# Kernel optimization log

Hardware: AMD Instinct MI355X
Metric: run time of the kernel (lower is better)

## Reference

```python
import jax, jax.numpy as jnp
import numpy as np

B, S, D = 4, 2048, 2048
NQ, NKV = 16, 4
HD = D // NQ          # head_size = 128
GROUP = NQ // NKV     # 4


def _rope_table(seq_len, head_size, theta=10000.0):
    # [seq, head_size/2, 2] = (cos, sin), matching torch polar freqs_cis
    inv = 1.0 / (theta ** (np.arange(0, head_size, 2, dtype=np.float32) / head_size))
    ang = np.arange(seq_len, dtype=np.float32)[:, None] * inv[None, :]
    return jnp.asarray(np.stack([np.cos(ang), np.sin(ang)], axis=-1))


def setup_inputs() -> dict:
    key = jax.random.key(0)
    ks = jax.random.split(key, 6)
    sd = 0.02
    return {
        "x": jax.random.normal(ks[0], (B, S, D), jnp.float32),
        "freq_cis": _rope_table(S, HD),
        "Wq": jax.random.normal(ks[1], (D, NQ * HD), jnp.float32) * sd,
        "bq": jnp.zeros((NQ * HD,), jnp.float32),
        "Wk": jax.random.normal(ks[2], (D, NKV * HD), jnp.float32) * sd,
        "bk": jnp.zeros((NKV * HD,), jnp.float32),
        "Wv": jax.random.normal(ks[3], (D, NKV * HD), jnp.float32) * sd,
        "bv": jnp.zeros((NKV * HD,), jnp.float32),
        "Wo": jax.random.normal(ks[4], (NQ * HD, D), jnp.float32) * sd,
        "start_pos": 0,
    }


def _apply_rope(x, fc):
    # x: [b, s, h, d]; fc: [s, d/2, 2] -> complex multiply on (even, odd) pairs
    xr = x.reshape(*x.shape[:-1], -1, 2)
    cos = fc[None, :, None, :, 0]
    sin = fc[None, :, None, :, 1]
    x0, x1 = xr[..., 0], xr[..., 1]
    out = jnp.stack([x0 * cos - x1 * sin, x0 * sin + x1 * cos], axis=-1)
    return out.reshape(x.shape)


def reference(x, freq_cis, Wq, bq, Wk, bk, Wv, bv, Wo, start_pos):
    b, s, _ = x.shape
    q = (x @ Wq + bq).reshape(b, s, NQ, HD)
    k = (x @ Wk + bk).reshape(b, s, NKV, HD)
    v = (x @ Wv + bv).reshape(b, s, NKV, HD)

    fc = freq_cis[start_pos:start_pos + s]
    q = _apply_rope(q, fc)
    k = _apply_rope(k, fc)

    # [b, nkv, group, s, d] query view; k/v stay [b, nkv, s, d] (GQA broadcast)
    q = q.transpose(0, 2, 1, 3).reshape(b, NKV, GROUP, s, HD)
    k = k.transpose(0, 2, 1, 3)
    v = v.transpose(0, 2, 1, 3)

    scale = 1.0 / jnp.sqrt(jnp.asarray(HD, x.dtype))
    scores = jnp.einsum("bhgqd,bhkd->bhgqk", q, k) * scale
    causal = jnp.tril(jnp.ones((s, s), bool))
    scores = jnp.where(causal[None, None, None], scores, jnp.asarray(-jnp.inf, scores.dtype))
    probs = jax.nn.softmax(scores, axis=-1)
    o = jnp.einsum("bhgqk,bhkd->bhgqd", probs, v)

    o = o.reshape(b, NQ, s, HD).transpose(0, 2, 1, 3).reshape(b, s, NQ * HD)
    return o @ Wo
```

## Files before the change

kernel.cpp:

```cpp
#include <hip/hip_runtime.h>
#include <stdint.h>

typedef __attribute__((ext_vector_type(8))) short bf16x8;
typedef __attribute__((ext_vector_type(4))) float f32x4;
typedef __attribute__((ext_vector_type(16))) float f32x16;

#define S_LEN 2048
#define D_MODEL 2048
#define NQH 16
#define NKVH 4
#define HDIM 128
#define BATCH 4

__device__ __forceinline__ float bf2f(unsigned short s) {
  union { unsigned u; float f; } v; v.u = ((unsigned)s) << 16; return v.f;
}
__device__ __forceinline__ unsigned short f2bf(float f) {
  union { float f; unsigned u; } v; v.f = f;
  unsigned r = v.u + 0x7FFFu + ((v.u >> 16) & 1u);
  return (unsigned short)(r >> 16);
}
__device__ __forceinline__ f32x4 fzero() {
  f32x4 v; v[0]=0.f; v[1]=0.f; v[2]=0.f; v[3]=0.f; return v;
}
__device__ __forceinline__ void async16(const void* g, void* l) {
  __builtin_amdgcn_global_load_lds(
      (const __attribute__((address_space(1))) unsigned int*)g,
      (__attribute__((address_space(3))) unsigned int*)l, 16, 0, 0);
}
__device__ __forceinline__ unsigned cvtpk(float lo, float hi) {
  unsigned r;
  asm("v_cvt_pk_bf16_f32 %0, %1, %2" : "=v"(r) : "v"(lo), "v"(hi));
  return r;
}

__global__ void k_convert_x(const float* __restrict__ x, unsigned short* __restrict__ xb, int n4) {
  int stride = gridDim.x * blockDim.x;
  for (int i = blockIdx.x * blockDim.x + threadIdx.x; i < n4; i += stride) {
    float4 v = ((const float4*)x)[i];
    ushort4 o;
    o.x = f2bf(v.x); o.y = f2bf(v.y); o.z = f2bf(v.z); o.w = f2bf(v.w);
    ((ushort4*)xb)[i] = o;
  }
}

__global__ void k_transpose_convert(const float* __restrict__ W, unsigned short* __restrict__ Wt,
                                    int K, int N) {
  __shared__ float tile[32][33];
  int tx = threadIdx.x & 31, ty = threadIdx.x >> 5;
  int n0 = blockIdx.x * 32, k0 = blockIdx.y * 32;
  #pragma unroll
  for (int i = 0; i < 4; ++i)
    tile[ty + i*8][tx] = W[(size_t)(k0 + ty + i*8) * N + n0 + tx];
  __syncthreads();
  #pragma unroll
  for (int i = 0; i < 4; ++i)
    Wt[(size_t)(n0 + ty + i*8) * K + k0 + tx] = f2bf(tile[tx][ty + i*8]);
}

__global__ void k_transpose_bf16(const unsigned short* __restrict__ src,
                                 unsigned short* __restrict__ dst, int R, int C) {
  __shared__ unsigned short tile[32][33];
  int tx = threadIdx.x & 31, ty = threadIdx.x >> 5;
  int c0 = blockIdx.x * 32, r0 = blockIdx.y * 32;
  const unsigned short* s = src + (size_t)blockIdx.z * R * C;
  unsigned short* d = dst + (size_t)blockIdx.z * R * C;
  #pragma unroll
  for (int i = 0; i < 4; ++i)
    tile[ty + i*8][tx] = s[(size_t)(r0 + ty + i*8) * C + c0 + tx];
  __syncthreads();
  #pragma unroll
  for (int i = 0; i < 4; ++i)
    d[(size_t)(c0 + ty + i*8) * R + r0 + tx] = tile[tx][ty + i*8];
}

__global__ void k_rope(unsigned short* __restrict__ T, const float* __restrict__ fc,
                       const int* __restrict__ start_pos, int total) {
  int sp = start_pos[0];
  int stride = gridDim.x * blockDim.x;
  for (int i = blockIdx.x * blockDim.x + threadIdx.x; i < total; i += stride) {
    int d2 = i & 63;
    int s = (i >> 6) & (S_LEN - 1);
    unsigned v = ((const unsigned*)T)[i];
    float x0 = bf2f((unsigned short)(v & 0xFFFFu));
    float x1 = bf2f((unsigned short)(v >> 16));
    float c  = fc[((size_t)(sp + s) * 64 + d2) * 2];
    float sn = fc[((size_t)(sp + s) * 64 + d2) * 2 + 1];
    float y0 = x0 * c - x1 * sn;
    float y1 = x0 * sn + x1 * c;
    ((unsigned*)T)[i] = (unsigned)f2bf(y0) | ((unsigned)f2bf(y1) << 16);
  }
}


__device__ __forceinline__ bf16x8 ldsrd(const unsigned short* L, int row, int kk, int g) {
  int Xs = (kk * 64 + g * 16) ^ ((row & 7) << 4);
  return *(const bf16x8*)&L[row * 64 + (Xs >> 1)];
}
__device__ __forceinline__ void stage8(const unsigned short* __restrict__ G, int gbase,
                                       int k0, unsigned short* lds, int rowbase, int lane) {
  int row = rowbase + (lane >> 3);
  int col8 = (lane & 7) ^ ((lane >> 3) & 7);
  async16(G + (size_t)(gbase + row) * 2048 + k0 + col8 * 8, lds + rowbase * 64 + lane * 8);
}

#define BARRIER() __builtin_amdgcn_s_barrier()
#define LGKM0()  do { asm volatile("s_waitcnt lgkmcnt(0)" ::: "memory"); \
                      __builtin_amdgcn_sched_barrier(0); } while (0)
#define VMCNT4() asm volatile("s_waitcnt vmcnt(4)" ::: "memory")

template<int EPI>
__global__ __launch_bounds__(512, 2) void k_gemm256(
    const unsigned short* __restrict__ A, const unsigned short* __restrict__ Bt,
    const float* __restrict__ bq, const float* __restrict__ bk, const float* __restrict__ bv,
    unsigned short* __restrict__ Qo, unsigned short* __restrict__ Ko, unsigned short* __restrict__ Vo,
    float* __restrict__ Cf, int NXT)
{
  __shared__ __align__(16) unsigned short Abuf[2][256 * 64];
  __shared__ __align__(16) unsigned short Bbuf[2][256 * 64];
  const int NT = 32;
  const int tid = threadIdx.x, lane = tid & 63, w = tid >> 6;
  const int lr = lane & 15, g = lane >> 4;
  const int wm = w >> 2, wn = w & 3;

  int nwg = NXT * 32;
  int cpx = nwg >> 3;
  int bid = blockIdx.x;
  int swz = (bid & 7) * cpx + (bid >> 3);
  const int by = swz / NXT, bx = swz % NXT;
  const int mbase = by * 256, nbase = bx * 256;

  #define ST_AQ02(tt) if ((tt) < NT) { unsigned short* L = Abuf[(tt) & 1]; int k0 = (tt) * 64; \
    _Pragma("unroll") for (int it = 0; it < 2; ++it) { int sub = it * 8 + w; \
      stage8(A, mbase, k0, L, (sub >> 3) * 128 + (sub & 7) * 8, lane); } }
  #define ST_AQ13(tt) if ((tt) < NT) { unsigned short* L = Abuf[(tt) & 1]; int k0 = (tt) * 64; \
    _Pragma("unroll") for (int it = 0; it < 2; ++it) { int sub = it * 8 + w; \
      stage8(A, mbase, k0, L, 64 + (sub >> 3) * 128 + (sub & 7) * 8, lane); } }
  #define ST_BS0(tt) if ((tt) < NT) { unsigned short* L = Bbuf[(tt) & 1]; int k0 = (tt) * 64; \
    _Pragma("unroll") for (int it = 0; it < 2; ++it) { int sub = it * 8 + w; \
      stage8(Bt, nbase, k0, L, (sub >> 2) * 64 + (sub & 3) * 8, lane); } }
  #define ST_BS1(tt) if ((tt) < NT) { unsigned short* L = Bbuf[(tt) & 1]; int k0 = (tt) * 64; \
    _Pragma("unroll") for (int it = 0; it < 2; ++it) { int sub = it * 8 + w; \
      stage8(Bt, nbase, k0, L, 32 + (sub >> 2) * 64 + (sub & 3) * 8, lane); } }

  f32x4 acc[8][4];
  #pragma unroll
  for (int m = 0; m < 8; ++m)
    #pragma unroll
    for (int n = 0; n < 4; ++n) acc[m][n] = fzero();

  ST_AQ02(0); ST_AQ13(0); ST_BS0(0); ST_BS1(0);
  ST_AQ02(1); ST_BS1(1);
  VMCNT4();
  BARRIER();

  bf16x8 a[2][4], b[2][2];

  for (int t = 0; t < NT; ++t) {
    const unsigned short* Al = Abuf[t & 1];
    const unsigned short* Bl = Bbuf[t & 1];

    #pragma unroll
    for (int kk = 0; kk < 2; ++kk) {
      #pragma unroll
      for (int m = 0; m < 4; ++m) a[kk][m] = ldsrd(Al, wm * 128 + m * 16 + lr, kk, g);
      #pragma unroll
      for (int n = 0; n < 2; ++n) b[kk][n] = ldsrd(Bl, wn * 64 + n * 16 + lr, kk, g);
    }
    ST_AQ13(t + 1);
    BARRIER(); LGKM0();
    __builtin_amdgcn_s_setprio(1);
    #pragma unroll
    for (int kk = 0; kk < 2; ++kk)
      #pragma unroll
      for (int m = 0; m < 4; ++m)
        #pragma unroll
        for (int n = 0; n < 2; ++n)
          acc[m][n] = __builtin_amdgcn_mfma_f32_16x16x32_bf16(a[kk][m], b[kk][n], acc[m][n], 0, 0, 0);
    __builtin_amdgcn_s_setprio(0);
    BARRIER();

    #pragma unroll
    for (int kk = 0; kk < 2; ++kk)
      #pragma unroll
      for (int n = 0; n < 2; ++n) b[kk][n] = ldsrd(Bl, wn * 64 + (2 + n) * 16 + lr, kk, g);
    ST_BS0(t + 1);
    BARRIER(); LGKM0();
    __builtin_amdgcn_s_setprio(1);
    #pragma unroll
    for (int kk = 0; kk < 2; ++kk)
      #pragma unroll
      for (int m = 0; m < 4; ++m)
        #pragma unroll
        for (int n = 0; n < 2; ++n)
          acc[m][2 + n] = __builtin_amdgcn_mfma_f32_16x16x32_bf16(a[kk][m], b[kk][n], acc[m][2 + n], 0, 0, 0);
    __builtin_amdgcn_s_setprio(0);
    BARRIER();

    #pragma unroll
    for (int kk = 0; kk < 2; ++kk)
      #pragma unroll
      for (int m = 0; m < 4; ++m) a[kk][m] = ldsrd(Al, wm * 128 + 64 + m * 16 + lr, kk, g);
    ST_AQ02(t + 2);
    BARRIER(); LGKM0();
    __builtin_amdgcn_s_setprio(1);
    #pragma unroll
    for (int kk = 0; kk < 2; ++kk)
      #pragma unroll
      for (int m = 0; m < 4; ++m)
        #pragma unroll
        for (int n = 0; n < 2; ++n)
          acc[4 + m][2 + n] = __builtin_amdgcn_mfma_f32_16x16x32_bf16(a[kk][m], b[kk][n], acc[4 + m][2 + n], 0, 0, 0);
    __builtin_amdgcn_s_setprio(0);
    BARRIER();

    #pragma unroll
    for (int kk = 0; kk < 2; ++kk)
      #pragma unroll
      for (int n = 0; n < 2; ++n) b[kk][n] = ldsrd(Bl, wn * 64 + n * 16 + lr, kk, g);
    ST_BS1(t + 2);
    VMCNT4();
    BARRIER(); LGKM0();
    __builtin_amdgcn_s_setprio(1);
    #pragma unroll
    for (int kk = 0; kk < 2; ++kk)
      #pragma unroll
      for (int m = 0; m < 4; ++m)
        #pragma unroll
        for (int n = 0; n < 2; ++n)
          acc[4 + m][n] = __builtin_amdgcn_mfma_f32_16x16x32_bf16(a[kk][m], b[kk][n], acc[4 + m][n], 0, 0, 0);
    __builtin_amdgcn_s_setprio(0);
    BARRIER();
  }

  #pragma unroll
  for (int m = 0; m < 8; ++m)
    #pragma unroll
    for (int n = 0; n < 4; ++n)
      #pragma unroll
      for (int i = 0; i < 4; ++i) {
        int mg = mbase + wm * 128 + m * 16 + g * 4 + i;
        int ng = nbase + wn * 64 + n * 16 + lr;
        float val = acc[m][n][i];
        if (EPI == 1) {
          Cf[(size_t)mg * 2048 + ng] = val;
        } else {
          int bb = mg >> 11, s = mg & 2047;
          if (ng < 2048) {
            val += bq[ng];
            int h = ng >> 7, d = ng & 127;
            Qo[((size_t)(bb * NQH + h) * S_LEN + s) * HDIM + d] = f2bf(val);
          } else if (ng < 2560) {
            int nn = ng - 2048;
            val += bk[nn];
            int h = nn >> 7, d = nn & 127;
            Ko[((size_t)(bb * NKVH + h) * S_LEN + s) * HDIM + d] = f2bf(val);
          } else {
            int nn = ng - 2560;
            val += bv[nn];
            int h = nn >> 7, d = nn & 127;
            Vo[((size_t)(bb * NKVH + h) * S_LEN + s) * HDIM + d] = f2bf(val);
          }
        }
      }
  #undef ST_AQ02
  #undef ST_AQ13
  #undef ST_BS0
  #undef ST_BS1
}

__global__ __launch_bounds__(512, 2) void k_flash2(
    const unsigned short* __restrict__ Q, const unsigned short* __restrict__ K,
    const unsigned short* __restrict__ Vt, unsigned short* __restrict__ O)
{
  __shared__ __align__(16) unsigned short SH[32768];

  const int tid = threadIdx.x;
  const int lane = tid & 63;
  const int w = tid >> 6;
  const int ql = lane & 31;
  const int hi = lane >> 5;

  const int bh = blockIdx.x >> 2;
  const int tp = blockIdx.x & 3;
  const int b = bh >> 4, h = bh & 15;
  const int kh = h >> 2;

  const unsigned short* Qbase = Q + (size_t)(b * NQH + h) * S_LEN * HDIM;
  const unsigned short* Kbase = K + (size_t)(b * NKVH + kh) * S_LEN * HDIM;
  const unsigned short* Vtb   = Vt + (size_t)(b * NKVH + kh) * HDIM * S_LEN;

  const float scale = 0.08838834764831845f;

  #pragma unroll 1
  for (int half = 0; half < 2; ++half) {
    const int t = half ? (7 - tp) : tp;
    const int nkv = 4 * t + 4;
    const int qg = t * 256 + w * 32 + ql;

    __syncthreads();

    bf16x8 qf[8];
    {
      const unsigned short* qp = Qbase + (size_t)qg * HDIM;
      #pragma unroll
      for (int dd = 0; dd < 8; ++dd)
        qf[dd] = *(const bf16x8*)(qp + dd * 16 + hi * 8);
    }

    float m_r = -1e30f, l_r = 0.f;
    f32x16 oA[4];
    #pragma unroll
    for (int db = 0; db < 4; ++db)
      #pragma unroll
      for (int r = 0; r < 16; ++r) oA[db][r] = 0.f;

    {
      unsigned short* Kd = SH;
      unsigned short* Vd = SH + 16384;
      #pragma unroll
      for (int it = 0; it < 2; ++it) {
        int c = tid + it * 512;
        int row = c >> 4, col = c & 15;
        int lcol = (col & 8) | ((col ^ (row & 7)) & 7);
        async16(Kbase + (size_t)row * HDIM + lcol * 8, Kd + c * 8);
      }
      #pragma unroll
      for (int it = 0; it < 2; ++it) {
        int c = tid + it * 512;
        int row = c >> 3, col = c & 7;
        int lcol = col ^ (row & 7);
        async16(Vtb + (size_t)row * S_LEN + lcol * 8, Vd + c * 8);
      }
    }
    __syncthreads();

    for (int j = 0; j < nkv; ++j) {
      const int cur = j & 1;
      const unsigned short* Kl = SH + cur * 8192;
      const unsigned short* Vl = SH + 16384 + cur * 8192;

      if (j + 1 < nkv) {
        unsigned short* Kd = SH + (cur ^ 1) * 8192;
        unsigned short* Vd = SH + 16384 + (cur ^ 1) * 8192;
        #pragma unroll
        for (int it = 0; it < 2; ++it) {
          int c = tid + it * 512;
          int row = c >> 4, col = c & 15;
          int lcol = (col & 8) | ((col ^ (row & 7)) & 7);
          async16(Kbase + (size_t)((j + 1) * 64 + row) * HDIM + lcol * 8, Kd + c * 8);
        }
        #pragma unroll
        for (int it = 0; it < 2; ++it) {
          int c = tid + it * 512;
          int row = c >> 3, col = c & 7;
          int lcol = col ^ (row & 7);
          async16(Vtb + (size_t)row * S_LEN + (j + 1) * 64 + lcol * 8, Vd + c * 8);
        }
      }

      if (j * 64 <= t * 256 + w * 32 + 31) {
        f32x16 p0, p1;
        #pragma unroll
        for (int r = 0; r < 16; ++r) { p0[r] = 0.f; p1[r] = 0.f; }
        #pragma unroll
        for (int dd = 0; dd < 8; ++dd) {
          const int off = (((dd * 32 + hi * 16) ^ ((ql & 7) << 4)) >> 1);
          bf16x8 a0 = *(const bf16x8*)&Kl[ql * 128 + off];
          bf16x8 a1 = *(const bf16x8*)&Kl[(32 + ql) * 128 + off];
          p0 = __builtin_amdgcn_mfma_f32_32x32x16_bf16(a0, qf[dd], p0, 0, 0, 0);
          p1 = __builtin_amdgcn_mfma_f32_32x32x16_bf16(a1, qf[dd], p1, 0, 0, 0);
        }

        #pragma unroll
        for (int r = 0; r < 16; ++r) {
          const int kl = (r & 3) + 8 * (r >> 2);
          int kg = j * 64 + kl + 4 * hi;
          p0[r] = (kg > qg) ? -1e30f : p0[r] * scale;
          p1[r] = (kg + 32 > qg) ? -1e30f : p1[r] * scale;
        }

        float pm = -1e30f;
        #pragma unroll
        for (int r = 0; r < 16; ++r) pm = fmaxf(pm, fmaxf(p0[r], p1[r]));
        pm = fmaxf(pm, __shfl_xor(pm, 32));
        const float mn = fmaxf(m_r, pm);
        const float corr = __expf(m_r - mn);
        m_r = mn;
        float rs = 0.f;
        #pragma unroll
        for (int r = 0; r < 16; ++r) {
          p0[r] = __expf(p0[r] - mn);
          p1[r] = __expf(p1[r] - mn);
          rs += p0[r] + p1[r];
        }
        rs += __shfl_xor(rs, 32);
        l_r = l_r * corr + rs;
        #pragma unroll
        for (int db = 0; db < 4; ++db)
          #pragma unroll
          for (int r = 0; r < 16; ++r) oA[db][r] *= corr;

        bf16x8 pb[4];
        {
          unsigned Wv[8], W2v[8];
          #pragma unroll
          for (int d = 0; d < 4; ++d) {
            Wv[d]      = cvtpk(p0[4*d],     p0[4*d + 1]);
            W2v[d]     = cvtpk(p0[4*d + 2], p0[4*d + 3]);
            Wv[4 + d]  = cvtpk(p1[4*d],     p1[4*d + 1]);
            W2v[4 + d] = cvtpk(p1[4*d + 2], p1[4*d + 3]);
          }
          #pragma unroll
          for (int kt = 0; kt < 2; ++kt) {
            #pragma unroll
            for (int s = 0; s < 2; ++s) {
              unsigned ownW   = hi ? Wv[kt*4 + 2*s + 1]  : Wv[kt*4 + 2*s];
              unsigned sendW  = hi ? Wv[kt*4 + 2*s]      : Wv[kt*4 + 2*s + 1];
              unsigned recvW  = (unsigned)__shfl_xor((int)sendW, 32);
              unsigned ownW2  = hi ? W2v[kt*4 + 2*s + 1] : W2v[kt*4 + 2*s];
              unsigned sendW2 = hi ? W2v[kt*4 + 2*s]     : W2v[kt*4 + 2*s + 1];
              unsigned recvW2 = (unsigned)__shfl_xor((int)sendW2, 32);
              union { unsigned u[4]; bf16x8 v; } pk;
              pk.u[0] = hi ? recvW  : ownW;
              pk.u[1] = hi ? recvW2 : ownW2;
              pk.u[2] = hi ? ownW   : recvW;
              pk.u[3] = hi ? ownW2  : recvW2;
              pb[kt*2 + s] = pk.v;
            }
          }
        }

        #pragma unroll
        for (int ks = 0; ks < 4; ++ks) {
          #pragma unroll
          for (int db = 0; db < 4; ++db) {
            const int off = (((ks * 32 + hi * 16) ^ ((ql & 7) << 4)) >> 1);
            bf16x8 av = *(const bf16x8*)&Vl[(db * 32 + ql) * 64 + off];
            oA[db] = __builtin_amdgcn_mfma_f32_32x32x16_bf16(av, pb[ks], oA[db], 0, 0, 0);
          }
        }
      }
      __syncthreads();
    }

    {
      const float invl = 1.f / l_r;
      const int qloc = w * 32 + ql;
      #pragma unroll
      for (int db = 0; db < 4; ++db)
        #pragma unroll
        for (int g4 = 0; g4 < 4; ++g4) {
          unsigned lo  = cvtpk(oA[db][g4*4 + 0] * invl, oA[db][g4*4 + 1] * invl);
          unsigned hi2 = cvtpk(oA[db][g4*4 + 2] * invl, oA[db][g4*4 + 3] * invl);
          int byteoff = qloc * 256 + ((db * 64 + g4 * 16 + hi * 8) ^ ((qloc & 7) << 4));
          *(uint2*)((char*)SH + byteoff) = make_uint2(lo, hi2);
        }
    }
    __syncthreads();
    {
      const int q2 = tid >> 1, hf = tid & 1;
      unsigned short* orow = O + ((size_t)(b * S_LEN + t * 256 + q2)) * D_MODEL + h * HDIM + hf * 64;
      #pragma unroll
      for (int u = 0; u < 8; ++u) {
        int byteoff = q2 * 256 + ((hf * 128 + u * 16) ^ ((q2 & 7) << 4));
        bf16x8 v = *(const bf16x8*)((const char*)SH + byteoff);
        *(bf16x8*)(orow + u * 8) = v;
      }
    }
  }
}

extern "C" void kernel_launch(void* const* d_in, const int* in_sizes, int n_in,
                              void* d_out, int out_size, void* d_ws, size_t ws_size,
                              hipStream_t stream) {
  (void)in_sizes; (void)n_in; (void)out_size; (void)ws_size;
  const float* x  = (const float*)d_in[0];
  const float* fc = (const float*)d_in[1];
  const float* Wq = (const float*)d_in[2];
  const float* bq = (const float*)d_in[3];
  const float* Wk = (const float*)d_in[4];
  const float* bk = (const float*)d_in[5];
  const float* Wv = (const float*)d_in[6];
  const float* bv = (const float*)d_in[7];
  const float* Wo = (const float*)d_in[8];
  const int* start_pos = (const int*)d_in[9];
  float* out = (float*)d_out;

  unsigned short* ws = (unsigned short*)d_ws;
  size_t off = 0;
  unsigned short* xb  = ws + off; off += (size_t)8192 * 2048;
  unsigned short* Wt  = ws + off; off += (size_t)3072 * 2048;
  unsigned short* Wot = ws + off; off += (size_t)2048 * 2048;
  unsigned short* Qb  = ws + off; off += (size_t)BATCH * NQH  * S_LEN * HDIM;
  unsigned short* Kb  = ws + off; off += (size_t)BATCH * NKVH * S_LEN * HDIM;
  unsigned short* Vb  = ws + off; off += (size_t)BATCH * NKVH * S_LEN * HDIM;
  unsigned short* Vtb = ws + off; off += (size_t)BATCH * NKVH * S_LEN * HDIM;
  unsigned short* Ob  = ws + off; off += (size_t)8192 * 2048;

  k_convert_x<<<2048, 256, 0, stream>>>(x, xb, 8192 * 2048 / 4);
  k_transpose_convert<<<dim3(64, 64), 256, 0, stream>>>(Wq, Wt, 2048, 2048);
  k_transpose_convert<<<dim3(16, 64), 256, 0, stream>>>(Wk, Wt + (size_t)2048 * 2048, 2048, 512);
  k_transpose_convert<<<dim3(16, 64), 256, 0, stream>>>(Wv, Wt + (size_t)2560 * 2048, 2048, 512);
  k_transpose_convert<<<dim3(64, 64), 256, 0, stream>>>(Wo, Wot, 2048, 2048);

  k_gemm256<0><<<dim3(384), 512, 0, stream>>>(xb, Wt, bq, bk, bv, Qb, Kb, Vb, nullptr, 12);

  k_rope<<<2048, 256, 0, stream>>>(Qb, fc, start_pos, BATCH * NQH * S_LEN * 64);
  k_rope<<<2048, 256, 0, stream>>>(Kb, fc, start_pos, BATCH * NKVH * S_LEN * 64);
  k_transpose_bf16<<<dim3(4, 64, 16), 256, 0, stream>>>(Vb, Vtb, S_LEN, HDIM);

  k_flash2<<<dim3(256), 512, 0, stream>>>(Qb, Kb, Vtb, Ob);

  k_gemm256<1><<<dim3(256), 512, 0, stream>>>(Ob, Wot, nullptr, nullptr, nullptr,
                                              nullptr, nullptr, nullptr, out, 8);
}
```

Measured before the change: 385.8 us.

## Shrink GEMM tile to 256x128 with triple-buffered LDS pipeline

Replaces the 256x256 GEMM tile with a 256x128 tile, which doubles the number of workgroups for both the QKV projection and the output projection. The LDS staging moves from two buffers to three, prefetching two K-steps ahead with simpler whole-tile async loads, and each K-step now uses two MFMA phases instead of four. The aim is better CU occupancy and load balance on 256 CUs (384 and 256 blocks previously), at the cost of lower arithmetic intensity per tile and more global/L2 traffic for A.

```diff
diff --git a/kernel.cpp b/kernel.cpp
--- a/kernel.cpp
+++ b/kernel.cpp
@@ -97,27 +97,22 @@
   int Xs = (kk * 64 + g * 16) ^ ((row & 7) << 4);
   return *(const bf16x8*)&L[row * 64 + (Xs >> 1)];
 }
-__device__ __forceinline__ void stage8(const unsigned short* __restrict__ G, int gbase,
-                                       int k0, unsigned short* lds, int rowbase, int lane) {
-  int row = rowbase + (lane >> 3);
-  int col8 = (lane & 7) ^ ((lane >> 3) & 7);
-  async16(G + (size_t)(gbase + row) * 2048 + k0 + col8 * 8, lds + rowbase * 64 + lane * 8);
-}
 
 #define BARRIER() __builtin_amdgcn_s_barrier()
 #define LGKM0()  do { asm volatile("s_waitcnt lgkmcnt(0)" ::: "memory"); \
                       __builtin_amdgcn_sched_barrier(0); } while (0)
-#define VMCNT4() asm volatile("s_waitcnt vmcnt(4)" ::: "memory")
+#define VMCNT6() asm volatile("s_waitcnt vmcnt(6)" ::: "memory")
+#define VMCNT0() asm volatile("s_waitcnt vmcnt(0)" ::: "memory")
 
 template<int EPI>
-__global__ __launch_bounds__(512, 2) void k_gemm256(
+__global__ __launch_bounds__(512, 2) void k_gemm128(
     const unsigned short* __restrict__ A, const unsigned short* __restrict__ Bt,
     const float* __restrict__ bq, const float* __restrict__ bk, const float* __restrict__ bv,
     unsigned short* __restrict__ Qo, unsigned short* __restrict__ Ko, unsigned short* __restrict__ Vo,
     float* __restrict__ Cf, int NXT)
 {
-  __shared__ __align__(16) unsigned short Abuf[2][256 * 64];
-  __shared__ __align__(16) unsigned short Bbuf[2][256 * 64];
+  __shared__ __align__(16) unsigned short Ab[3][256 * 64];
+  __shared__ __align__(16) unsigned short Bb[3][128 * 64];
   const int NT = 32;
   const int tid = threadIdx.x, lane = tid & 63, w = tid >> 6;
   const int lr = lane & 15, g = lane >> 4;
@@ -128,46 +123,40 @@
   int bid = blockIdx.x;
   int swz = (bid & 7) * cpx + (bid >> 3);
   const int by = swz / NXT, bx = swz % NXT;
-  const int mbase = by * 256, nbase = bx * 256;
-
-  #define ST_AQ02(tt) if ((tt) < NT) { unsigned short* L = Abuf[(tt) & 1]; int k0 = (tt) * 64; \
-    _Pragma("unroll") for (int it = 0; it < 2; ++it) { int sub = it * 8 + w; \
-      stage8(A, mbase, k0, L, (sub >> 3) * 128 + (sub & 7) * 8, lane); } }
-  #define ST_AQ13(tt) if ((tt) < NT) { unsigned short* L = Abuf[(tt) & 1]; int k0 = (tt) * 64; \
-    _Pragma("unroll") for (int it = 0; it < 2; ++it) { int sub = it * 8 + w; \
-      stage8(A, mbase, k0, L, 64 + (sub >> 3) * 128 + (sub & 7) * 8, lane); } }
-  #define ST_BS0(tt) if ((tt) < NT) { unsigned short* L = Bbuf[(tt) & 1]; int k0 = (tt) * 64; \
-    _Pragma("unroll") for (int it = 0; it < 2; ++it) { int sub = it * 8 + w; \
-      stage8(Bt, nbase, k0, L, (sub >> 2) * 64 + (sub & 3) * 8, lane); } }
-  #define ST_BS1(tt) if ((tt) < NT) { unsigned short* L = Bbuf[(tt) & 1]; int k0 = (tt) * 64; \
-    _Pragma("unroll") for (int it = 0; it < 2; ++it) { int sub = it * 8 + w; \
-      stage8(Bt, nbase, k0, L, 32 + (sub >> 2) * 64 + (sub & 3) * 8, lane); } }
-
-  f32x4 acc[8][4];
+  const int mbase = by * 256, nbase = bx * 128;
+
+  #define ST_A(tt) { unsigned short* L = Ab[(tt) % 3]; int k0 = (tt) * 64; \
+    _Pragma("unroll") for (int it = 0; it < 4; ++it) { int c = tid + it * 512; \
+      int row = c >> 3, col8 = (c & 7) ^ (row & 7); \
+      async16(A + (size_t)(mbase + row) * 2048 + k0 + col8 * 8, L + c * 8); } }
+  #define ST_B(tt) { unsigned short* L = Bb[(tt) % 3]; int k0 = (tt) * 64; \
+    _Pragma("unroll") for (int it = 0; it < 2; ++it) { int c = tid + it * 512; \
+      int row = c >> 3, col8 = (c & 7) ^ (row & 7); \
+      async16(Bt + (size_t)(nbase + row) * 2048 + k0 + col8 * 8, L + c * 8); } }
+
+  f32x4 acc[8][2];
   #pragma unroll
   for (int m = 0; m < 8; ++m)
     #pragma unroll
-    for (int n = 0; n < 4; ++n) acc[m][n] = fzero();
-
-  ST_AQ02(0); ST_AQ13(0); ST_BS0(0); ST_BS1(0);
-  ST_AQ02(1); ST_BS1(1);
-  VMCNT4();
+    for (int n = 0; n < 2; ++n) acc[m][n] = fzero();
+
+  ST_A(0); ST_B(0); ST_A(1); ST_B(1);
+  VMCNT6();
   BARRIER();
 
-  bf16x8 a[2][4], b[2][2];
-
   for (int t = 0; t < NT; ++t) {
-    const unsigned short* Al = Abuf[t & 1];
-    const unsigned short* Bl = Bbuf[t & 1];
+    const unsigned short* Al = Ab[t % 3];
+    const unsigned short* Bl = Bb[t % 3];
+    bf16x8 a[2][4], b[2][2];
 
     #pragma unroll
     for (int kk = 0; kk < 2; ++kk) {
       #pragma unroll
       for (int m = 0; m < 4; ++m) a[kk][m] = ldsrd(Al, wm * 128 + m * 16 + lr, kk, g);
       #pragma unroll
-      for (int n = 0; n < 2; ++n) b[kk][n] = ldsrd(Bl, wn * 64 + n * 16 + lr, kk, g);
-    }
-    ST_AQ13(t + 1);
+      for (int n = 0; n < 2; ++n) b[kk][n] = ldsrd(Bl, wn * 32 + n * 16 + lr, kk, g);
+    }
+    if (t + 2 < NT) ST_A(t + 2);
     BARRIER(); LGKM0();
     __builtin_amdgcn_s_setprio(1);
     #pragma unroll
@@ -183,43 +172,8 @@
     #pragma unroll
     for (int kk = 0; kk < 2; ++kk)
       #pragma unroll
-      for (int n = 0; n < 2; ++n) b[kk][n] = ldsrd(Bl, wn * 64 + (2 + n) * 16 + lr, kk, g);
-    ST_BS0(t + 1);
-    BARRIER(); LGKM0();
-    __builtin_amdgcn_s_setprio(1);
-    #pragma unroll
-    for (int kk = 0; kk < 2; ++kk)
-      #pragma unroll
-      for (int m = 0; m < 4; ++m)
-        #pragma unroll
-        for (int n = 0; n < 2; ++n)
-          acc[m][2 + n] = __builtin_amdgcn_mfma_f32_16x16x32_bf16(a[kk][m], b[kk][n], acc[m][2 + n], 0, 0, 0);
-    __builtin_amdgcn_s_setprio(0);
-    BARRIER();
-
-    #pragma unroll
-    for (int kk = 0; kk < 2; ++kk)
-      #pragma unroll
       for (int m = 0; m < 4; ++m) a[kk][m] = ldsrd(Al, wm * 128 + 64 + m * 16 + lr, kk, g);
-    ST_AQ02(t + 2);
-    BARRIER(); LGKM0();
-    __builtin_amdgcn_s_setprio(1);
-    #pragma unroll
-    for (int kk = 0; kk < 2; ++kk)
-      #pragma unroll
-      for (int m = 0; m < 4; ++m)
-        #pragma unroll
-        for (int n = 0; n < 2; ++n)
-          acc[4 + m][2 + n] = __builtin_amdgcn_mfma_f32_16x16x32_bf16(a[kk][m], b[kk][n], acc[4 + m][2 + n], 0, 0, 0);
-    __builtin_amdgcn_s_setprio(0);
-    BARRIER();
-
-    #pragma unroll
-    for (int kk = 0; kk < 2; ++kk)
-      #pragma unroll
-      for (int n = 0; n < 2; ++n) b[kk][n] = ldsrd(Bl, wn * 64 + n * 16 + lr, kk, g);
-    ST_BS1(t + 2);
-    VMCNT4();
+    if (t + 2 < NT) { ST_B(t + 2); VMCNT6(); } else { VMCNT0(); }
     BARRIER(); LGKM0();
     __builtin_amdgcn_s_setprio(1);
     #pragma unroll
@@ -236,11 +190,11 @@
   #pragma unroll
   for (int m = 0; m < 8; ++m)
     #pragma unroll
-    for (int n = 0; n < 4; ++n)
+    for (int n = 0; n < 2; ++n)
       #pragma unroll
       for (int i = 0; i < 4; ++i) {
-        int mg = mbase + wm * 128 + m * 16 + g * 4 + i;
-        int ng = nbase + wn * 64 + n * 16 + lr;
+        int mg = mbase + wm * 128 + (m >> 2) * 64 + (m & 3) * 16 + g * 4 + i;
+        int ng = nbase + wn * 32 + n * 16 + lr;
         float val = acc[m][n][i];
         if (EPI == 1) {
           Cf[(size_t)mg * 2048 + ng] = val;
@@ -263,10 +217,8 @@
           }
         }
       }
-  #undef ST_AQ02
-  #undef ST_AQ13
-  #undef ST_BS0
-  #undef ST_BS1
+  #undef ST_A
+  #undef ST_B
 }
 
 __global__ __launch_bounds__(512, 2) void k_flash2(
@@ -504,7 +456,7 @@
   k_transpose_convert<<<dim3(16, 64), 256, 0, stream>>>(Wv, Wt + (size_t)2560 * 2048, 2048, 512);
   k_transpose_convert<<<dim3(64, 64), 256, 0, stream>>>(Wo, Wot, 2048, 2048);
 
-  k_gemm256<0><<<dim3(384), 512, 0, stream>>>(xb, Wt, bq, bk, bv, Qb, Kb, Vb, nullptr, 12);
+  k_gemm128<0><<<dim3(768), 512, 0, stream>>>(xb, Wt, bq, bk, bv, Qb, Kb, Vb, nullptr, 24);
 
   k_rope<<<2048, 256, 0, stream>>>(Qb, fc, start_pos, BATCH * NQH * S_LEN * 64);
   k_rope<<<2048, 256, 0, stream>>>(Kb, fc, start_pos, BATCH * NKVH * S_LEN * 64);
@@ -512,6 +464,6 @@
 
   k_flash2<<<dim3(256), 512, 0, stream>>>(Qb, Kb, Vtb, Ob);
 
-  k_gemm256<1><<<dim3(256), 512, 0, stream>>>(Ob, Wot, nullptr, nullptr, nullptr,
-                                              nullptr, nullptr, nullptr, out, 8);
-}
+  k_gemm128<1><<<dim3(512), 512, 0, stream>>>(Ob, Wot, nullptr, nullptr, nullptr,
+                                              nullptr, nullptr, nullptr, out, 16);
+}
```

Result: slower. 394.5 us (+2.3%).

## Fuse RoPE into QKV GEMM epilogue and retile it to 256x128 with triple buffering

Applied to the files above, without the earlier changes.

Removes the two standalone RoPE kernels by applying the rotation in the QKV GEMM epilogue, pairing even and odd lanes with a shuffle. This avoids an extra read-modify-write pass over Q and K in global memory. The QKV GEMM is also rewritten with a 256x128 tile, 768 workgroups and a three-stage LDS ring, replacing the earlier 256x256 double-buffered schedule. The output GEMM becomes its own non-templated kernel. The trade-off is a smaller tile with less data reuse per workgroup, plus more LDS use that could limit occupancy.

```diff
diff --git a/kernel.cpp b/kernel.cpp
--- a/kernel.cpp
+++ b/kernel.cpp
@@ -74,24 +74,12 @@
     d[(size_t)(c0 + ty + i*8) * R + r0 + tx] = tile[tx][ty + i*8];
 }
 
-__global__ void k_rope(unsigned short* __restrict__ T, const float* __restrict__ fc,
-                       const int* __restrict__ start_pos, int total) {
-  int sp = start_pos[0];
-  int stride = gridDim.x * blockDim.x;
-  for (int i = blockIdx.x * blockDim.x + threadIdx.x; i < total; i += stride) {
-    int d2 = i & 63;
-    int s = (i >> 6) & (S_LEN - 1);
-    unsigned v = ((const unsigned*)T)[i];
-    float x0 = bf2f((unsigned short)(v & 0xFFFFu));
-    float x1 = bf2f((unsigned short)(v >> 16));
-    float c  = fc[((size_t)(sp + s) * 64 + d2) * 2];
-    float sn = fc[((size_t)(sp + s) * 64 + d2) * 2 + 1];
-    float y0 = x0 * c - x1 * sn;
-    float y1 = x0 * sn + x1 * c;
-    ((unsigned*)T)[i] = (unsigned)f2bf(y0) | ((unsigned)f2bf(y1) << 16);
-  }
-}
-
+#define BARRIER() __builtin_amdgcn_s_barrier()
+#define LGKM0()  do { asm volatile("s_waitcnt lgkmcnt(0)" ::: "memory"); \
+                      __builtin_amdgcn_sched_barrier(0); } while (0)
+#define VMCNT6() asm volatile("s_waitcnt vmcnt(6)" ::: "memory")
+#define VMCNT4() asm volatile("s_waitcnt vmcnt(4)" ::: "memory")
+#define VMCNT0() asm volatile("s_waitcnt vmcnt(0)" ::: "memory")
 
 __device__ __forceinline__ bf16x8 ldsrd(const unsigned short* L, int row, int kk, int g) {
   int Xs = (kk * 64 + g * 16) ^ ((row & 7) << 4);
@@ -104,21 +92,129 @@
   async16(G + (size_t)(gbase + row) * 2048 + k0 + col8 * 8, lds + rowbase * 64 + lane * 8);
 }
 
-#define BARRIER() __builtin_amdgcn_s_barrier()
-#define LGKM0()  do { asm volatile("s_waitcnt lgkmcnt(0)" ::: "memory"); \
-                      __builtin_amdgcn_sched_barrier(0); } while (0)
-#define VMCNT4() asm volatile("s_waitcnt vmcnt(4)" ::: "memory")
-
-template<int EPI>
-__global__ __launch_bounds__(512, 2) void k_gemm256(
+__global__ __launch_bounds__(512, 2) void k_gemm_qkv(
     const unsigned short* __restrict__ A, const unsigned short* __restrict__ Bt,
     const float* __restrict__ bq, const float* __restrict__ bk, const float* __restrict__ bv,
-    unsigned short* __restrict__ Qo, unsigned short* __restrict__ Ko, unsigned short* __restrict__ Vo,
-    float* __restrict__ Cf, int NXT)
+    const float* __restrict__ fc, const int* __restrict__ start_pos,
+    unsigned short* __restrict__ Qo, unsigned short* __restrict__ Ko, unsigned short* __restrict__ Vo)
+{
+  __shared__ __align__(16) unsigned short Ab[3][256 * 64];
+  __shared__ __align__(16) unsigned short Bb[3][128 * 64];
+  const int NT = 32, NXT = 24;
+  const int tid = threadIdx.x, lane = tid & 63, w = tid >> 6;
+  const int lr = lane & 15, g = lane >> 4;
+  const int wm = w >> 2, wn = w & 3;
+
+  int nwg = NXT * 32;
+  int cpx = nwg >> 3;
+  int bid = blockIdx.x;
+  int swz = (bid & 7) * cpx + (bid >> 3);
+  const int by = swz / NXT, bx = swz % NXT;
+  const int mbase = by * 256, nbase = bx * 128;
+
+  #define ST_A(tt) { unsigned short* L = Ab[(tt) % 3]; int k0 = (tt) * 64; \
+    _Pragma("unroll") for (int it = 0; it < 4; ++it) { int c = tid + it * 512; \
+      int row = c >> 3, col8 = (c & 7) ^ (row & 7); \
+      async16(A + (size_t)(mbase + row) * 2048 + k0 + col8 * 8, L + c * 8); } }
+  #define ST_B(tt) { unsigned short* L = Bb[(tt) % 3]; int k0 = (tt) * 64; \
+    _Pragma("unroll") for (int it = 0; it < 2; ++it) { int c = tid + it * 512; \
+      int row = c >> 3, col8 = (c & 7) ^ (row & 7); \
+      async16(Bt + (size_t)(nbase + row) * 2048 + k0 + col8 * 8, L + c * 8); } }
+
+  f32x4 acc[8][2];
+  #pragma unroll
+  for (int m = 0; m < 8; ++m)
+    #pragma unroll
+    for (int n = 0; n < 2; ++n) acc[m][n] = fzero();
+
+  ST_A(0); ST_B(0); ST_A(1); ST_B(1);
+  VMCNT6();
+  BARRIER();
+
+  for (int t = 0; t < NT; ++t) {
+    const unsigned short* Al = Ab[t % 3];
+    const unsigned short* Bl = Bb[t % 3];
+    bf16x8 a[2][4], b[2][2];
+
+    #pragma unroll
+    for (int kk = 0; kk < 2; ++kk) {
+      #pragma unroll
+      for (int m = 0; m < 4; ++m) a[kk][m] = ldsrd(Al, wm * 128 + m * 16 + lr, kk, g);
+      #pragma unroll
+      for (int n = 0; n < 2; ++n) b[kk][n] = ldsrd(Bl, wn * 32 + n * 16 + lr, kk, g);
+    }
+    if (t + 2 < NT) ST_A(t + 2);
+    BARRIER(); LGKM0();
+    __builtin_amdgcn_s_setprio(1);
+    #pragma unroll
+    for (int kk = 0; kk < 2; ++kk)
+      #pragma unroll
+      for (int m = 0; m < 4; ++m)
+        #pragma unroll
+        for (int n = 0; n < 2; ++n)
+          acc[m][n] = __builtin_amdgcn_mfma_f32_16x16x32_bf16(a[kk][m], b[kk][n], acc[m][n], 0, 0, 0);
+    __builtin_amdgcn_s_setprio(0);
+    BARRIER();
+
+    #pragma unroll
+    for (int kk = 0; kk < 2; ++kk)
+      #pragma unroll
+      for (int m = 0; m < 4; ++m) a[kk][m] = ldsrd(Al, wm * 128 + 64 + m * 16 + lr, kk, g);
+    if (t + 2 < NT) { ST_B(t + 2); VMCNT6(); } else { VMCNT0(); }
+    BARRIER(); LGKM0();
+    __builtin_amdgcn_s_setprio(1);
+    #pragma unroll
+    for (int kk = 0; kk < 2; ++kk)
+      #pragma unroll
+      for (int m = 0; m < 4; ++m)
+        #pragma unroll
+        for (int n = 0; n < 2; ++n)
+          acc[4 + m][n] = __builtin_amdgcn_mfma_f32_16x16x32_bf16(a[kk][m], b[kk][n], acc[4 + m][n], 0, 0, 0);
+    __builtin_amdgcn_s_setprio(0);
+    BARRIER();
+  }
+
+  const int sp = start_pos[0];
+  #pragma unroll
+  for (int n = 0; n < 2; ++n) {
+    const int ng = nbase + wn * 32 + n * 16 + lr;
+    unsigned short* dst;
+    int NH; float bias;
+    if (ng < 2048)      { dst = Qo; NH = NQH;  bias = bq[ng]; }
+    else if (ng < 2560) { dst = Ko; NH = NKVH; bias = bk[ng - 2048]; }
+    else                { dst = Vo; NH = NKVH; bias = bv[ng - 2560]; }
+    const int hh = (ng < 2048 ? ng : (ng < 2560 ? ng - 2048 : ng - 2560)) >> 7;
+    const int dd = ng & 127;
+    const bool dorope = (ng < 2560);
+    const size_t hoff = (size_t)hh * S_LEN * HDIM + dd;
+    const int d2 = dd >> 1;
+    #pragma unroll
+    for (int m = 0; m < 8; ++m)
+      #pragma unroll
+      for (int i = 0; i < 4; ++i) {
+        int mg = mbase + wm * 128 + (m >> 2) * 64 + (m & 3) * 16 + g * 4 + i;
+        int bb = mg >> 11, s = mg & 2047;
+        float val = acc[m][n][i] + bias;
+        float other = __shfl_xor(val, 1);
+        if (dorope) {
+          float2 cs = *(const float2*)&fc[((size_t)(sp + s) * 64 + d2) * 2];
+          val = (dd & 1) ? fmaf(other, cs.y, val * cs.x)
+                         : (val * cs.x - other * cs.y);
+        }
+        dst[(size_t)bb * NH * S_LEN * HDIM + hoff + (size_t)s * HDIM] = f2bf(val);
+      }
+  }
+  #undef ST_A
+  #undef ST_B
+}
+
+__global__ __launch_bounds__(512, 2) void k_gemm_out256(
+    const unsigned short* __restrict__ A, const unsigned short* __restrict__ Bt,
+    float* __restrict__ Cf)
 {
   __shared__ __align__(16) unsigned short Abuf[2][256 * 64];
   __shared__ __align__(16) unsigned short Bbuf[2][256 * 64];
-  const int NT = 32;
+  const int NT = 32, NXT = 8;
   const int tid = threadIdx.x, lane = tid & 63, w = tid >> 6;
   const int lr = lane & 15, g = lane >> 4;
   const int wm = w >> 2, wn = w & 3;
@@ -241,27 +337,7 @@
       for (int i = 0; i < 4; ++i) {
         int mg = mbase + wm * 128 + m * 16 + g * 4 + i;
         int ng = nbase + wn * 64 + n * 16 + lr;
-        float val = acc[m][n][i];
-        if (EPI == 1) {
-          Cf[(size_t)mg * 2048 + ng] = val;
-        } else {
-          int bb = mg >> 11, s = mg & 2047;
-          if (ng < 2048) {
-            val += bq[ng];
-            int h = ng >> 7, d = ng & 127;
-            Qo[((size_t)(bb * NQH + h) * S_LEN + s) * HDIM + d] = f2bf(val);
-          } else if (ng < 2560) {
-            int nn = ng - 2048;
-            val += bk[nn];
-            int h = nn >> 7, d = nn & 127;
-            Ko[((size_t)(bb * NKVH + h) * S_LEN + s) * HDIM + d] = f2bf(val);
-          } else {
-            int nn = ng - 2560;
-            val += bv[nn];
-            int h = nn >> 7, d = nn & 127;
-            Vo[((size_t)(bb * NKVH + h) * S_LEN + s) * HDIM + d] = f2bf(val);
-          }
-        }
+        Cf[(size_t)mg * 2048 + ng] = acc[m][n][i];
       }
   #undef ST_AQ02
   #undef ST_AQ13
@@ -504,14 +580,11 @@
   k_transpose_convert<<<dim3(16, 64), 256, 0, stream>>>(Wv, Wt + (size_t)2560 * 2048, 2048, 512);
   k_transpose_convert<<<dim3(64, 64), 256, 0, stream>>>(Wo, Wot, 2048, 2048);
 
-  k_gemm256<0><<<dim3(384), 512, 0, stream>>>(xb, Wt, bq, bk, bv, Qb, Kb, Vb, nullptr, 12);
-
-  k_rope<<<2048, 256, 0, stream>>>(Qb, fc, start_pos, BATCH * NQH * S_LEN * 64);
-  k_rope<<<2048, 256, 0, stream>>>(Kb, fc, start_pos, BATCH * NKVH * S_LEN * 64);
+  k_gemm_qkv<<<dim3(768), 512, 0, stream>>>(xb, Wt, bq, bk, bv, fc, start_pos, Qb, Kb, Vb);
+
   k_transpose_bf16<<<dim3(4, 64, 16), 256, 0, stream>>>(Vb, Vtb, S_LEN, HDIM);
 
   k_flash2<<<dim3(256), 512, 0, stream>>>(Qb, Kb, Vtb, Ob);
 
-  k_gemm256<1><<<dim3(256), 512, 0, stream>>>(Ob, Wot, nullptr, nullptr, nullptr,
-                                              nullptr, nullptr, nullptr, out, 8);
-}
+  k_gemm_out256<<<dim3(256), 512, 0, stream>>>(Ob, Wot, out);
+}
```

New measurement: 389.5 us. About the same (+1.0%).
